# Optimization experiments

Hardware: AMD Instinct MI355X
Metric: run time of the kernel (lower is better)

## Reference

```python
import jax, jax.numpy as jnp
import numpy as np

N, E, D_IN, D_OUT, MAX_DEG = 50000, 800000, 128, 128, 64
ALPHA = 0.5


def _linear_params(key, fan_in, fan_out):
    s = 1.0 / np.sqrt(fan_in)
    kw, kb = jax.random.split(key)
    W = jax.random.uniform(kw, (fan_out, fan_in), jnp.float32, -s, s)
    b = jax.random.uniform(kb, (fan_out,), jnp.float32, -s, s)
    return W, b


def setup_inputs() -> dict:
    key = jax.random.key(0)
    ks = jax.random.split(key, 16)
    x = jax.random.normal(ks[0], (N, D_IN), jnp.float32)
    edge_index = jax.random.randint(ks[1], (2, E), 0, N, dtype=jnp.int64)
    in_degree = jax.random.randint(ks[2], (N,), 0, MAX_DEG, dtype=jnp.int64)
    out_degree = jax.random.randint(ks[3], (N,), 0, MAX_DEG, dtype=jnp.int64)
    out_deg_mask = jax.random.uniform(ks[4], (N,), jnp.float32)
    out_deg_mask_bias = jax.random.uniform(ks[5], (N,), jnp.float32)
    in_deg_mask = jax.random.uniform(ks[6], (N,), jnp.float32)
    in_deg_mask_bias = jax.random.uniform(ks[7], (N,), jnp.float32)
    W_src, b_src = _linear_params(ks[8], D_IN, D_OUT)
    W_dst, b_dst = _linear_params(ks[9], D_IN, D_OUT)
    W_out_f, b_out_f = _linear_params(ks[10], D_IN, 1)
    W_in_f, b_in_f = _linear_params(ks[11], D_IN, 1)
    W_fc, b_fc = _linear_params(ks[12], D_IN, D_OUT)
    # degree embedding tables, padding_idx=0 -> row 0 zeroed
    in_deg_table = (jax.random.normal(ks[13], (MAX_DEG, D_IN), jnp.float32)).at[0].set(0.0)
    out_deg_table = (jax.random.normal(ks[14], (MAX_DEG, D_IN), jnp.float32)).at[0].set(0.0)
    return {
        "x": x, "edge_index": edge_index,
        "in_degree": in_degree, "out_degree": out_degree,
        "out_deg_mask": out_deg_mask, "out_deg_mask_bias": out_deg_mask_bias,
        "in_deg_mask": in_deg_mask, "in_deg_mask_bias": in_deg_mask_bias,
        "W_src": W_src, "b_src": b_src, "W_dst": W_dst, "b_dst": b_dst,
        "W_out_f": W_out_f, "b_out_f": b_out_f, "W_in_f": W_in_f, "b_in_f": b_in_f,
        "W_fc": W_fc, "b_fc": b_fc,
        "in_deg_table": in_deg_table, "out_deg_table": out_deg_table,
    }


def reference(x, edge_index, in_degree, out_degree,
              out_deg_mask, out_deg_mask_bias, in_deg_mask, in_deg_mask_bias,
              W_src, b_src, W_dst, b_dst,
              W_out_f, b_out_f, W_in_f, b_in_f,
              W_fc, b_fc, in_deg_table, out_deg_table):
    n = x.shape[0]
    row, col = edge_index[0], edge_index[1]
    ones = jnp.ones(row.shape[0], x.dtype)
    # directed norm D_out^{-1/2} A D_in^{-1/2}; transpose reuses the same edge weights
    out_deg = jax.ops.segment_sum(ones, row, num_segments=n)
    in_deg = jax.ops.segment_sum(ones, col, num_segments=n)
    o_inv = jnp.where(out_deg > 0, jax.lax.rsqrt(jnp.maximum(out_deg, 1e-12)), 0.0)
    i_inv = jnp.where(in_deg > 0, jax.lax.rsqrt(jnp.maximum(in_deg, 1e-12)), 0.0)
    w = o_inv[row] * i_inv[col]  # [E]
    # adj_norm @ x and adj_t_norm @ x (SpMM via gather + segment_sum)
    out_nei = jax.ops.segment_sum(w[:, None] * x[col], row, num_segments=n)  # [N,D]
    in_nei = jax.ops.segment_sum(w[:, None] * x[row], col, num_segments=n)   # [N,D]
    # degree-gated filter
    c_out = (out_nei - x + out_deg_table[out_degree]) @ W_out_f.T + b_out_f  # [N,1]
    c_in = (in_nei - x + in_deg_table[in_degree]) @ W_in_f.T + b_in_f        # [N,1]
    C = jax.nn.softmax(jnp.concatenate([c_out, c_in], axis=1), axis=1)        # tau_softmax, tau=1
    C_out = C[:, 0:1] * out_deg_mask[:, None] + out_deg_mask_bias[:, None]
    C_in = C[:, 1:2] * in_deg_mask[:, None] + in_deg_mask_bias[:, None]
    out = (C_out * (out_nei @ W_src.T + b_src)
           + C_in * (in_nei @ W_dst.T + b_dst)
           + ALPHA * (x @ W_fc.T + b_fc))
    return out, C_in, C_out
```

## Files before the change

### kernel.cpp

```cpp
#include <hip/hip_runtime.h>

#define NN 50000
#define EE 800000
#define DD 128
#define CAP 48
#define MT 64
#define XSL 6250
#define PB 128

typedef short short8_t __attribute__((ext_vector_type(8)));
typedef float f32x4 __attribute__((ext_vector_type(4)));

__device__ __forceinline__ unsigned short f2bf(float f) {
    union { float f; unsigned int i; } v; v.f = f;
    unsigned int x = v.i;
    x += 0x7FFFu + ((x >> 16) & 1u);
    return (unsigned short)(x >> 16);
}
__device__ __forceinline__ unsigned int pack2(float a, float b) {
    return (unsigned int)f2bf(a) | ((unsigned int)f2bf(b) << 16);
}
__device__ __forceinline__ float2 bf2x2(unsigned int u) {
    union { unsigned int i; float f; } lo, hi;
    lo.i = u << 16;
    hi.i = u & 0xFFFF0000u;
    return make_float2(lo.f, hi.f);
}

__global__ void k_conv(const float* __restrict__ x,
                       const float* __restrict__ W_src,
                       const float* __restrict__ W_dst,
                       const float* __restrict__ W_fc,
                       unsigned short* __restrict__ xb,
                       unsigned short* __restrict__ wbf) {
    int t = blockIdx.x * 256 + threadIdx.x;
    int base = t * 4;
    if (base < NN * DD) {
        float4 v = *(const float4*)(x + base);
        uint2 p; p.x = pack2(v.x, v.y); p.y = pack2(v.z, v.w);
        *(uint2*)(xb + base) = p;
    } else {
        int b2 = base - NN * DD;
        if (b2 < 3 * 16384) {
            int src = b2 >> 14;
            int off = b2 & 16383;
            const float* W = (src == 0) ? W_src : (src == 1) ? W_dst : W_fc;
            float sc = (src == 2) ? 0.5f : 1.0f;
            float4 v = *(const float4*)(W + off);
            uint2 p; p.x = pack2(v.x * sc, v.y * sc); p.y = pack2(v.z * sc, v.w * sc);
            *(uint2*)(wbf + b2) = p;
        }
    }
}

__global__ void __launch_bounds__(256) k_place(
    const int* __restrict__ ei, int* __restrict__ cnt,
    unsigned short* __restrict__ bkt_row, unsigned short* __restrict__ bkt_col) {
    int xcd = blockIdx.x & 7;
    int b   = blockIdx.x >> 3;
    int lo = xcd * XSL, hi = lo + XSL;
    for (int e = b * 256 + threadIdx.x; e < EE; e += PB * 256) {
        int r = ei[e];
        int c = ei[EE + e];
        if (r >= lo && r < hi) {
            int po = atomicAdd(&cnt[r], 1);
            if (po < CAP) bkt_row[(size_t)r * CAP + po] = (unsigned short)c;
        }
        if (c >= lo && c < hi) {
            int pi = atomicAdd(&cnt[NN + c], 1);
            if (pi < CAP) bkt_col[(size_t)c * CAP + pi] = (unsigned short)r;
        }
    }
}

__global__ void k_inv(const int* __restrict__ cnt, float* __restrict__ inv) {
    int t = blockIdx.x * 256 + threadIdx.x;
    if (t >= 2 * NN) return;
    int d = cnt[t];
    inv[t] = (d > 0) ? (1.0f / sqrtf((float)d)) : 0.0f;
}

__global__ void __launch_bounds__(256) k_gather(
    const uint2* __restrict__ xb2, const float4* __restrict__ x4,
    const unsigned short* __restrict__ bkt_row, const unsigned short* __restrict__ bkt_col,
    const int* __restrict__ cnt,
    const float* __restrict__ o_inv, const float* __restrict__ i_inv,
    const int* __restrict__ in_degree, const int* __restrict__ out_degree,
    const float* __restrict__ odm, const float* __restrict__ odmb,
    const float* __restrict__ idm, const float* __restrict__ idmb,
    const float4* __restrict__ W_out_f4, const float* __restrict__ b_out_f,
    const float4* __restrict__ W_in_f4, const float* __restrict__ b_in_f,
    const float4* __restrict__ in_tab4, const float4* __restrict__ out_tab4,
    uint2* __restrict__ onb2, uint2* __restrict__ inb2,
    float* __restrict__ scbuf,
    float* __restrict__ outCin, float* __restrict__ outCout)
{
    __shared__ float4 sred[2][4][32];
    int half = threadIdx.x >> 7;
    int n = blockIdx.x * 2 + half;
    int t = threadIdx.x & 127;
    int g = t >> 5;
    int l = t & 31;

    float po_sum = 0.0f;

    float4 acc = make_float4(0.f, 0.f, 0.f, 0.f);
    {
        int deg = cnt[n]; deg = (deg > CAP) ? CAP : deg;
        const unsigned short* bp = bkt_row + (size_t)n * CAP;
        int j = g;
        for (; j + 12 < deg; j += 16) {
            int nb0 = bp[j], nb1 = bp[j + 4], nb2 = bp[j + 8], nb3 = bp[j + 12];
            float w0 = i_inv[nb0], w1 = i_inv[nb1], w2 = i_inv[nb2], w3 = i_inv[nb3];
            uint2 u0 = xb2[(size_t)nb0 * 32 + l];
            uint2 u1 = xb2[(size_t)nb1 * 32 + l];
            uint2 u2 = xb2[(size_t)nb2 * 32 + l];
            uint2 u3 = xb2[(size_t)nb3 * 32 + l];
            float2 p0 = bf2x2(u0.x), p1 = bf2x2(u0.y);
            float2 q0 = bf2x2(u1.x), q1 = bf2x2(u1.y);
            float2 r0 = bf2x2(u2.x), r1 = bf2x2(u2.y);
            float2 s0 = bf2x2(u3.x), s1 = bf2x2(u3.y);
            acc.x += w0 * p0.x + w1 * q0.x + w2 * r0.x + w3 * s0.x;
            acc.y += w0 * p0.y + w1 * q0.y + w2 * r0.y + w3 * s0.y;
            acc.z += w0 * p1.x + w1 * q1.x + w2 * r1.x + w3 * s1.x;
            acc.w += w0 * p1.y + w1 * q1.y + w2 * r1.y + w3 * s1.y;
        }
        for (; j + 4 < deg; j += 8) {
            int nb0 = bp[j], nb1 = bp[j + 4];
            float w0 = i_inv[nb0], w1 = i_inv[nb1];
            uint2 u0 = xb2[(size_t)nb0 * 32 + l];
            uint2 u1 = xb2[(size_t)nb1 * 32 + l];
            float2 p0 = bf2x2(u0.x), p1 = bf2x2(u0.y);
            float2 q0 = bf2x2(u1.x), q1 = bf2x2(u1.y);
            acc.x += w0 * p0.x + w1 * q0.x;
            acc.y += w0 * p0.y + w1 * q0.y;
            acc.z += w0 * p1.x + w1 * q1.x;
            acc.w += w0 * p1.y + w1 * q1.y;
        }
        if (j < deg) {
            int nb = bp[j];
            float w = i_inv[nb];
            uint2 u = xb2[(size_t)nb * 32 + l];
            float2 p0 = bf2x2(u.x), p1 = bf2x2(u.y);
            acc.x += w * p0.x; acc.y += w * p0.y; acc.z += w * p1.x; acc.w += w * p1.y;
        }
    }
    sred[half][g][l] = acc;
    __syncthreads();
    if (g == 0) {
        float4 a0 = sred[half][0][l], a1 = sred[half][1][l];
        float4 a2 = sred[half][2][l], a3 = sred[half][3][l];
        float wn = o_inv[n];
        float4 r;
        r.x = wn * (a0.x + a1.x + a2.x + a3.x);
        r.y = wn * (a0.y + a1.y + a2.y + a3.y);
        r.z = wn * (a0.z + a1.z + a2.z + a3.z);
        r.w = wn * (a0.w + a1.w + a2.w + a3.w);
        uint2 pw; pw.x = pack2(r.x, r.y); pw.y = pack2(r.z, r.w);
        onb2[(size_t)n * 32 + l] = pw;
        int odg = out_degree[n];
        odg = (odg < 0) ? 0 : (odg > 63 ? 63 : odg);
        float4 xv = x4[(size_t)n * 32 + l];
        float4 ot = out_tab4[(size_t)odg * 32 + l];
        float4 wf = W_out_f4[l];
        float po = (r.x - xv.x + ot.x) * wf.x + (r.y - xv.y + ot.y) * wf.y
                 + (r.z - xv.z + ot.z) * wf.z + (r.w - xv.w + ot.w) * wf.w;
        #pragma unroll
        for (int off = 16; off > 0; off >>= 1) po += __shfl_down(po, off);
        po_sum = po;
    }
    __syncthreads();

    acc = make_float4(0.f, 0.f, 0.f, 0.f);
    {
        int deg = cnt[NN + n]; deg = (deg > CAP) ? CAP : deg;
        const unsigned short* bp = bkt_col + (size_t)n * CAP;
        int j = g;
        for (; j + 12 < deg; j += 16) {
            int nb0 = bp[j], nb1 = bp[j + 4], nb2 = bp[j + 8], nb3 = bp[j + 12];
            float w0 = o_inv[nb0], w1 = o_inv[nb1], w2 = o_inv[nb2], w3 = o_inv[nb3];
            uint2 u0 = xb2[(size_t)nb0 * 32 + l];
            uint2 u1 = xb2[(size_t)nb1 * 32 + l];
            uint2 u2 = xb2[(size_t)nb2 * 32 + l];
            uint2 u3 = xb2[(size_t)nb3 * 32 + l];
            float2 p0 = bf2x2(u0.x), p1 = bf2x2(u0.y);
            float2 q0 = bf2x2(u1.x), q1 = bf2x2(u1.y);
            float2 r0 = bf2x2(u2.x), r1 = bf2x2(u2.y);
            float2 s0 = bf2x2(u3.x), s1 = bf2x2(u3.y);
            acc.x += w0 * p0.x + w1 * q0.x + w2 * r0.x + w3 * s0.x;
            acc.y += w0 * p0.y + w1 * q0.y + w2 * r0.y + w3 * s0.y;
            acc.z += w0 * p1.x + w1 * q1.x + w2 * r1.x + w3 * s1.x;
            acc.w += w0 * p1.y + w1 * q1.y + w2 * r1.y + w3 * s1.y;
        }
        for (; j + 4 < deg; j += 8) {
            int nb0 = bp[j], nb1 = bp[j + 4];
            float w0 = o_inv[nb0], w1 = o_inv[nb1];
            uint2 u0 = xb2[(size_t)nb0 * 32 + l];
            uint2 u1 = xb2[(size_t)nb1 * 32 + l];
            float2 p0 = bf2x2(u0.x), p1 = bf2x2(u0.y);
            float2 q0 = bf2x2(u1.x), q1 = bf2x2(u1.y);
            acc.x += w0 * p0.x + w1 * q0.x;
            acc.y += w0 * p0.y + w1 * q0.y;
            acc.z += w0 * p1.x + w1 * q1.x;
            acc.w += w0 * p1.y + w1 * q1.y;
        }
        if (j < deg) {
            int nb = bp[j];
            float w = o_inv[nb];
            uint2 u = xb2[(size_t)nb * 32 + l];
            float2 p0 = bf2x2(u.x), p1 = bf2x2(u.y);
            acc.x += w * p0.x; acc.y += w * p0.y; acc.z += w * p1.x; acc.w += w * p1.y;
        }
    }
    sred[half][g][l] = acc;
    __syncthreads();
    if (g == 0) {
        float4 a0 = sred[half][0][l], a1 = sred[half][1][l];
        float4 a2 = sred[half][2][l], a3 = sred[half][3][l];
        float wn = i_inv[n];
        float4 r;
        r.x = wn * (a0.x + a1.x + a2.x + a3.x);
        r.y = wn * (a0.y + a1.y + a2.y + a3.y);
        r.z = wn * (a0.z + a1.z + a2.z + a3.z);
        r.w = wn * (a0.w + a1.w + a2.w + a3.w);
        uint2 pw; pw.x = pack2(r.x, r.y); pw.y = pack2(r.z, r.w);
        inb2[(size_t)n * 32 + l] = pw;
        int idg = in_degree[n];
        idg = (idg < 0) ? 0 : (idg > 63 ? 63 : idg);
        float4 xv = x4[(size_t)n * 32 + l];
        float4 it = in_tab4[(size_t)idg * 32 + l];
        float4 wf = W_in_f4[l];
        float pi = (r.x - xv.x + it.x) * wf.x + (r.y - xv.y + it.y) * wf.y
                 + (r.z - xv.z + it.z) * wf.z + (r.w - xv.w + it.w) * wf.w;
        #pragma unroll
        for (int off = 16; off > 0; off >>= 1) pi += __shfl_down(pi, off);
        if (l == 0) {
            float c_out = po_sum + b_out_f[0];
            float c_in  = pi + b_in_f[0];
            float m  = fmaxf(c_out, c_in);
            float eo = expf(c_out - m);
            float e2 = expf(c_in  - m);
            float inv = 1.0f / (eo + e2);
            float Cout = (eo * inv) * odm[n] + odmb[n];
            float Cin  = (e2 * inv) * idm[n] + idmb[n];
            scbuf[2 * n]     = Cout;
            scbuf[2 * n + 1] = Cin;
            outCin[n]  = Cin;
            outCout[n] = Cout;
        }
    }
}

__global__ void __launch_bounds__(256) k_gemm(
    const unsigned int* __restrict__ xb32,
    const unsigned int* __restrict__ onb32, const unsigned int* __restrict__ inb32,
    const unsigned short* __restrict__ wbf,
    const float* __restrict__ b_src, const float* __restrict__ b_dst,
    const float* __restrict__ b_fc,
    const float* __restrict__ scbuf,
    float* __restrict__ out)
{
    __shared__ unsigned short sA[MT * 72];
    __shared__ unsigned short sBt[DD * 72];

    int tid = threadIdx.x;
    int wid = tid >> 6;
    int lane = tid & 63;
    int ml = lane & 15;
    int kq = lane >> 4;
    int n0 = blockIdx.x * MT;

    f32x4 accv[8];
    #pragma unroll
    for (int i = 0; i < 8; i++) accv[i] = (f32x4)0.0f;

    const unsigned int* srcs[3] = { onb32, inb32, xb32 };

    for (int kt = 0; kt < 6; kt++) {
        int srcsel = kt >> 1;
        int k0 = (kt & 1) * 64;
        const unsigned int* S = srcs[srcsel];

        #pragma unroll
        for (int r = 0; r < 2; r++) {
            int s = tid + 256 * r;
            int row = s >> 3;
            int cg = s & 7;
            int gn = n0 + row;
            uint4 p = make_uint4(0u, 0u, 0u, 0u);
            if (gn < NN) {
                uint4 u = *(const uint4*)(S + (size_t)gn * 64 + (k0 >> 1) + cg * 4);
                if (srcsel == 2) {
                    p = u;
                } else {
                    float sc = scbuf[2 * gn + srcsel];
                    float2 a = bf2x2(u.x), b = bf2x2(u.y), c = bf2x2(u.z), d = bf2x2(u.w);
                    p.x = pack2(a.x * sc, a.y * sc);
                    p.y = pack2(b.x * sc, b.y * sc);
                    p.z = pack2(c.x * sc, c.y * sc);
                    p.w = pack2(d.x * sc, d.y * sc);
                }
            }
            *(uint4*)(sA + row * 72 + cg * 8) = p;
        }
        #pragma unroll
        for (int r = 0; r < 4; r++) {
            int s = tid + 256 * r;
            int row = s >> 3;
            int cg = s & 7;
            uint4 w = *(const uint4*)(wbf + srcsel * 16384 + row * DD + k0 + cg * 8);
            *(uint4*)(sBt + row * 72 + cg * 8) = w;
        }
        __syncthreads();

        #pragma unroll
        for (int ks = 0; ks < 64; ks += 32) {
            short8_t a = *(const short8_t*)(sA + (16 * wid + ml) * 72 + ks + kq * 8);
            #pragma unroll
            for (int i = 0; i < 8; i++) {
                short8_t b = *(const short8_t*)(sBt + (16 * i + ml) * 72 + ks + kq * 8);
                accv[i] = __builtin_amdgcn_mfma_f32_16x16x32_bf16(a, b, accv[i], 0, 0, 0);
            }
        }
        __syncthreads();
    }

    int row_base = n0 + 16 * wid + 4 * kq;
    #pragma unroll
    for (int r = 0; r < 4; r++) {
        int row = row_base + r;
        if (row >= NN) continue;
        float Cout = scbuf[2 * row];
        float Cin  = scbuf[2 * row + 1];
        #pragma unroll
        for (int i = 0; i < 8; i++) {
            int col = 16 * i + ml;
            out[(size_t)row * DD + col] =
                accv[i][r] + Cout * b_src[col] + Cin * b_dst[col] + 0.5f * b_fc[col];
        }
    }
}

extern "C" void kernel_launch(void* const* d_in, const int* in_sizes, int n_in,
                              void* d_out, int out_size, void* d_ws, size_t ws_size,
                              hipStream_t stream) {
    const float* x    = (const float*)d_in[0];
    const int* ei     = (const int*)d_in[1];
    const int* in_degree  = (const int*)d_in[2];
    const int* out_degree = (const int*)d_in[3];
    const float* odm  = (const float*)d_in[4];
    const float* odmb = (const float*)d_in[5];
    const float* idm  = (const float*)d_in[6];
    const float* idmb = (const float*)d_in[7];
    const float* W_src = (const float*)d_in[8];
    const float* b_src = (const float*)d_in[9];
    const float* W_dst = (const float*)d_in[10];
    const float* b_dst = (const float*)d_in[11];
    const float* W_out_f = (const float*)d_in[12];
    const float* b_out_f = (const float*)d_in[13];
    const float* W_in_f  = (const float*)d_in[14];
    const float* b_in_f  = (const float*)d_in[15];
    const float* W_fc    = (const float*)d_in[16];
    const float* b_fc    = (const float*)d_in[17];
    const float* in_tab  = (const float*)d_in[18];
    const float* out_tab = (const float*)d_in[19];

    unsigned short* xb  = (unsigned short*)d_ws;
    unsigned short* onb = xb + (size_t)NN * DD;
    unsigned short* inb = onb + (size_t)NN * DD;
    float* scbuf = (float*)(inb + (size_t)NN * DD);
    float* invb  = scbuf + 2 * NN;
    unsigned short* wbf = (unsigned short*)(invb + 2 * NN);
    int* cnt     = (int*)(wbf + 3 * 16384);
    unsigned short* bkt_row = (unsigned short*)(cnt + 2 * NN);
    unsigned short* bkt_col = bkt_row + (size_t)NN * CAP;

    hipMemsetAsync(cnt, 0, (size_t)2 * NN * sizeof(int), stream);

    int conv_quads = (NN * DD + 3 * 16384) / 4;
    k_conv<<<(conv_quads + 255) / 256, 256, 0, stream>>>(x, W_src, W_dst, W_fc, xb, wbf);
    k_place<<<8 * PB, 256, 0, stream>>>(ei, cnt, bkt_row, bkt_col);
    k_inv<<<(2 * NN + 255) / 256, 256, 0, stream>>>(cnt, invb);

    float* o_inv = invb;
    float* i_inv = invb + NN;
    float* out_p  = (float*)d_out;
    float* cin_p  = out_p + (size_t)NN * DD;
    float* cout_p = cin_p + NN;

    k_gather<<<NN / 2, 256, 0, stream>>>((const uint2*)xb, (const float4*)x,
                                         bkt_row, bkt_col, cnt,
                                         o_inv, i_inv, in_degree, out_degree,
                                         odm, odmb, idm, idmb,
                                         (const float4*)W_out_f, b_out_f,
                                         (const float4*)W_in_f, b_in_f,
                                         (const float4*)in_tab, (const float4*)out_tab,
                                         (uint2*)onb, (uint2*)inb,
                                         scbuf, cin_p, cout_p);

    k_gemm<<<(NN + MT - 1) / MT, 256, 0, stream>>>(
        (const unsigned int*)xb, (const unsigned int*)onb, (const unsigned int*)inb,
        wbf, b_src, b_dst, b_fc, scbuf, out_p);
}
```

Before: 297.7 us.

## Gather both edge directions concurrently and pre-scale neighbor sums by gates

The gather kernel now gives two warp-groups to each direction (out-neighbors and in-neighbors) so both SpMM gathers run at once instead of one after the other, with deeper unrolling to keep eight loads in flight. The softmax gates are computed in shared memory and applied to the aggregated rows before the bf16 store. The GEMM loader can then copy the A tiles straight through without unpacking, scaling and repacking. The gather has more syncs and less per-group parallelism within each direction, and the gate scaling now happens before bf16 rounding instead of after, which changes rounding slightly.

```diff
diff --git a/kernel.cpp b/kernel.cpp
--- a/kernel.cpp
+++ b/kernel.cpp
@@ -96,158 +96,140 @@
     float* __restrict__ outCin, float* __restrict__ outCout)
 {
     __shared__ float4 sred[2][4][32];
+    __shared__ float sg[2][2];
+    __shared__ float sC[2][2];
     int half = threadIdx.x >> 7;
     int n = blockIdx.x * 2 + half;
     int t = threadIdx.x & 127;
     int g = t >> 5;
     int l = t & 31;
-
-    float po_sum = 0.0f;
+    int dir = g >> 1;
+    int gd  = g & 1;
+
+    const unsigned short* bp = ((dir == 0) ? bkt_row : bkt_col) + (size_t)n * CAP;
+    const float* wnb = (dir == 0) ? i_inv : o_inv;
+    int deg = cnt[dir * NN + n]; deg = (deg > CAP) ? CAP : deg;
 
     float4 acc = make_float4(0.f, 0.f, 0.f, 0.f);
-    {
-        int deg = cnt[n]; deg = (deg > CAP) ? CAP : deg;
-        const unsigned short* bp = bkt_row + (size_t)n * CAP;
-        int j = g;
-        for (; j + 12 < deg; j += 16) {
-            int nb0 = bp[j], nb1 = bp[j + 4], nb2 = bp[j + 8], nb3 = bp[j + 12];
-            float w0 = i_inv[nb0], w1 = i_inv[nb1], w2 = i_inv[nb2], w3 = i_inv[nb3];
-            uint2 u0 = xb2[(size_t)nb0 * 32 + l];
-            uint2 u1 = xb2[(size_t)nb1 * 32 + l];
-            uint2 u2 = xb2[(size_t)nb2 * 32 + l];
-            uint2 u3 = xb2[(size_t)nb3 * 32 + l];
-            float2 p0 = bf2x2(u0.x), p1 = bf2x2(u0.y);
-            float2 q0 = bf2x2(u1.x), q1 = bf2x2(u1.y);
-            float2 r0 = bf2x2(u2.x), r1 = bf2x2(u2.y);
-            float2 s0 = bf2x2(u3.x), s1 = bf2x2(u3.y);
-            acc.x += w0 * p0.x + w1 * q0.x + w2 * r0.x + w3 * s0.x;
-            acc.y += w0 * p0.y + w1 * q0.y + w2 * r0.y + w3 * s0.y;
-            acc.z += w0 * p1.x + w1 * q1.x + w2 * r1.x + w3 * s1.x;
-            acc.w += w0 * p1.y + w1 * q1.y + w2 * r1.y + w3 * s1.y;
-        }
-        for (; j + 4 < deg; j += 8) {
-            int nb0 = bp[j], nb1 = bp[j + 4];
-            float w0 = i_inv[nb0], w1 = i_inv[nb1];
-            uint2 u0 = xb2[(size_t)nb0 * 32 + l];
-            uint2 u1 = xb2[(size_t)nb1 * 32 + l];
-            float2 p0 = bf2x2(u0.x), p1 = bf2x2(u0.y);
-            float2 q0 = bf2x2(u1.x), q1 = bf2x2(u1.y);
-            acc.x += w0 * p0.x + w1 * q0.x;
-            acc.y += w0 * p0.y + w1 * q0.y;
-            acc.z += w0 * p1.x + w1 * q1.x;
-            acc.w += w0 * p1.y + w1 * q1.y;
-        }
-        if (j < deg) {
-            int nb = bp[j];
-            float w = i_inv[nb];
-            uint2 u = xb2[(size_t)nb * 32 + l];
-            float2 p0 = bf2x2(u.x), p1 = bf2x2(u.y);
-            acc.x += w * p0.x; acc.y += w * p0.y; acc.z += w * p1.x; acc.w += w * p1.y;
-        }
-    }
+    int j = gd;
+    for (; j + 14 < deg; j += 16) {
+        int nb0 = bp[j],      nb1 = bp[j + 2],  nb2_ = bp[j + 4],  nb3 = bp[j + 6];
+        int nb4 = bp[j + 8],  nb5 = bp[j + 10], nb6 = bp[j + 12],  nb7 = bp[j + 14];
+        float w0 = wnb[nb0], w1 = wnb[nb1], w2 = wnb[nb2_], w3 = wnb[nb3];
+        float w4 = wnb[nb4], w5 = wnb[nb5], w6 = wnb[nb6],  w7 = wnb[nb7];
+        uint2 u0 = xb2[(size_t)nb0 * 32 + l];
+        uint2 u1 = xb2[(size_t)nb1 * 32 + l];
+        uint2 u2 = xb2[(size_t)nb2_ * 32 + l];
+        uint2 u3 = xb2[(size_t)nb3 * 32 + l];
+        uint2 u4 = xb2[(size_t)nb4 * 32 + l];
+        uint2 u5 = xb2[(size_t)nb5 * 32 + l];
+        uint2 u6 = xb2[(size_t)nb6 * 32 + l];
+        uint2 u7 = xb2[(size_t)nb7 * 32 + l];
+        float2 p0 = bf2x2(u0.x), p1 = bf2x2(u0.y);
+        float2 q0 = bf2x2(u1.x), q1 = bf2x2(u1.y);
+        float2 r0 = bf2x2(u2.x), r1 = bf2x2(u2.y);
+        float2 s0 = bf2x2(u3.x), s1 = bf2x2(u3.y);
+        float2 t0 = bf2x2(u4.x), t1 = bf2x2(u4.y);
+        float2 v0 = bf2x2(u5.x), v1 = bf2x2(u5.y);
+        float2 y0 = bf2x2(u6.x), y1 = bf2x2(u6.y);
+        float2 z0 = bf2x2(u7.x), z1 = bf2x2(u7.y);
+        acc.x += w0 * p0.x + w1 * q0.x + w2 * r0.x + w3 * s0.x
+               + w4 * t0.x + w5 * v0.x + w6 * y0.x + w7 * z0.x;
+        acc.y += w0 * p0.y + w1 * q0.y + w2 * r0.y + w3 * s0.y
+               + w4 * t0.y + w5 * v0.y + w6 * y0.y + w7 * z0.y;
+        acc.z += w0 * p1.x + w1 * q1.x + w2 * r1.x + w3 * s1.x
+               + w4 * t1.x + w5 * v1.x + w6 * y1.x + w7 * z1.x;
+        acc.w += w0 * p1.y + w1 * q1.y + w2 * r1.y + w3 * s1.y
+               + w4 * t1.y + w5 * v1.y + w6 * y1.y + w7 * z1.y;
+    }
+    for (; j + 6 < deg; j += 8) {
+        int nb0 = bp[j], nb1 = bp[j + 2], nb2_ = bp[j + 4], nb3 = bp[j + 6];
+        float w0 = wnb[nb0], w1 = wnb[nb1], w2 = wnb[nb2_], w3 = wnb[nb3];
+        uint2 u0 = xb2[(size_t)nb0 * 32 + l];
+        uint2 u1 = xb2[(size_t)nb1 * 32 + l];
+        uint2 u2 = xb2[(size_t)nb2_ * 32 + l];
+        uint2 u3 = xb2[(size_t)nb3 * 32 + l];
+        float2 p0 = bf2x2(u0.x), p1 = bf2x2(u0.y);
+        float2 q0 = bf2x2(u1.x), q1 = bf2x2(u1.y);
+        float2 r0 = bf2x2(u2.x), r1 = bf2x2(u2.y);
+        float2 s0 = bf2x2(u3.x), s1 = bf2x2(u3.y);
+        acc.x += w0 * p0.x + w1 * q0.x + w2 * r0.x + w3 * s0.x;
+        acc.y += w0 * p0.y + w1 * q0.y + w2 * r0.y + w3 * s0.y;
+        acc.z += w0 * p1.x + w1 * q1.x + w2 * r1.x + w3 * s1.x;
+        acc.w += w0 * p1.y + w1 * q1.y + w2 * r1.y + w3 * s1.y;
+    }
+    for (; j + 2 < deg; j += 4) {
+        int nb0 = bp[j], nb1 = bp[j + 2];
+        float w0 = wnb[nb0], w1 = wnb[nb1];
+        uint2 u0 = xb2[(size_t)nb0 * 32 + l];
+        uint2 u1 = xb2[(size_t)nb1 * 32 + l];
+        float2 p0 = bf2x2(u0.x), p1 = bf2x2(u0.y);
+        float2 q0 = bf2x2(u1.x), q1 = bf2x2(u1.y);
+        acc.x += w0 * p0.x + w1 * q0.x;
+        acc.y += w0 * p0.y + w1 * q0.y;
+        acc.z += w0 * p1.x + w1 * q1.x;
+        acc.w += w0 * p1.y + w1 * q1.y;
+    }
+    if (j < deg) {
+        int nb = bp[j];
+        float w = wnb[nb];
+        uint2 u = xb2[(size_t)nb * 32 + l];
+        float2 p0 = bf2x2(u.x), p1 = bf2x2(u.y);
+        acc.x += w * p0.x; acc.y += w * p0.y; acc.z += w * p1.x; acc.w += w * p1.y;
+    }
+
     sred[half][g][l] = acc;
     __syncthreads();
-    if (g == 0) {
-        float4 a0 = sred[half][0][l], a1 = sred[half][1][l];
-        float4 a2 = sred[half][2][l], a3 = sred[half][3][l];
-        float wn = o_inv[n];
-        float4 r;
-        r.x = wn * (a0.x + a1.x + a2.x + a3.x);
-        r.y = wn * (a0.y + a1.y + a2.y + a3.y);
-        r.z = wn * (a0.z + a1.z + a2.z + a3.z);
-        r.w = wn * (a0.w + a1.w + a2.w + a3.w);
-        uint2 pw; pw.x = pack2(r.x, r.y); pw.y = pack2(r.z, r.w);
-        onb2[(size_t)n * 32 + l] = pw;
-        int odg = out_degree[n];
-        odg = (odg < 0) ? 0 : (odg > 63 ? 63 : odg);
+
+    float4 r = make_float4(0.f, 0.f, 0.f, 0.f);
+    if (gd == 0) {
+        float4 a0 = sred[half][dir * 2][l];
+        float4 a1 = sred[half][dir * 2 + 1][l];
+        float wn = (dir == 0) ? o_inv[n] : i_inv[n];
+        r.x = wn * (a0.x + a1.x);
+        r.y = wn * (a0.y + a1.y);
+        r.z = wn * (a0.z + a1.z);
+        r.w = wn * (a0.w + a1.w);
         float4 xv = x4[(size_t)n * 32 + l];
-        float4 ot = out_tab4[(size_t)odg * 32 + l];
-        float4 wf = W_out_f4[l];
-        float po = (r.x - xv.x + ot.x) * wf.x + (r.y - xv.y + ot.y) * wf.y
-                 + (r.z - xv.z + ot.z) * wf.z + (r.w - xv.w + ot.w) * wf.w;
-        #pragma unroll
-        for (int off = 16; off > 0; off >>= 1) po += __shfl_down(po, off);
-        po_sum = po;
+        float4 tb, wf;
+        if (dir == 0) {
+            int odg = out_degree[n];
+            odg = (odg < 0) ? 0 : (odg > 63 ? 63 : odg);
+            tb = out_tab4[(size_t)odg * 32 + l];
+            wf = W_out_f4[l];
+        } else {
+            int idg = in_degree[n];
+            idg = (idg < 0) ? 0 : (idg > 63 ? 63 : idg);
+            tb = in_tab4[(size_t)idg * 32 + l];
+            wf = W_in_f4[l];
+        }
+        float p = (r.x - xv.x + tb.x) * wf.x + (r.y - xv.y + tb.y) * wf.y
+                + (r.z - xv.z + tb.z) * wf.z + (r.w - xv.w + tb.w) * wf.w;
+        #pragma unroll
+        for (int off = 16; off > 0; off >>= 1) p += __shfl_down(p, off);
+        if (l == 0) sg[half][dir] = p;
     }
     __syncthreads();
-
-    acc = make_float4(0.f, 0.f, 0.f, 0.f);
-    {
-        int deg = cnt[NN + n]; deg = (deg > CAP) ? CAP : deg;
-        const unsigned short* bp = bkt_col + (size_t)n * CAP;
-        int j = g;
-        for (; j + 12 < deg; j += 16) {
-            int nb0 = bp[j], nb1 = bp[j + 4], nb2 = bp[j + 8], nb3 = bp[j + 12];
-            float w0 = o_inv[nb0], w1 = o_inv[nb1], w2 = o_inv[nb2], w3 = o_inv[nb3];
-            uint2 u0 = xb2[(size_t)nb0 * 32 + l];
-            uint2 u1 = xb2[(size_t)nb1 * 32 + l];
-            uint2 u2 = xb2[(size_t)nb2 * 32 + l];
-            uint2 u3 = xb2[(size_t)nb3 * 32 + l];
-            float2 p0 = bf2x2(u0.x), p1 = bf2x2(u0.y);
-            float2 q0 = bf2x2(u1.x), q1 = bf2x2(u1.y);
-            float2 r0 = bf2x2(u2.x), r1 = bf2x2(u2.y);
-            float2 s0 = bf2x2(u3.x), s1 = bf2x2(u3.y);
-            acc.x += w0 * p0.x + w1 * q0.x + w2 * r0.x + w3 * s0.x;
-            acc.y += w0 * p0.y + w1 * q0.y + w2 * r0.y + w3 * s0.y;
-            acc.z += w0 * p1.x + w1 * q1.x + w2 * r1.x + w3 * s1.x;
-            acc.w += w0 * p1.y + w1 * q1.y + w2 * r1.y + w3 * s1.y;
-        }
-        for (; j + 4 < deg; j += 8) {
-            int nb0 = bp[j], nb1 = bp[j + 4];
-            float w0 = o_inv[nb0], w1 = o_inv[nb1];
-            uint2 u0 = xb2[(size_t)nb0 * 32 + l];
-            uint2 u1 = xb2[(size_t)nb1 * 32 + l];
-            float2 p0 = bf2x2(u0.x), p1 = bf2x2(u0.y);
-            float2 q0 = bf2x2(u1.x), q1 = bf2x2(u1.y);
-            acc.x += w0 * p0.x + w1 * q0.x;
-            acc.y += w0 * p0.y + w1 * q0.y;
-            acc.z += w0 * p1.x + w1 * q1.x;
-            acc.w += w0 * p1.y + w1 * q1.y;
-        }
-        if (j < deg) {
-            int nb = bp[j];
-            float w = o_inv[nb];
-            uint2 u = xb2[(size_t)nb * 32 + l];
-            float2 p0 = bf2x2(u.x), p1 = bf2x2(u.y);
-            acc.x += w * p0.x; acc.y += w * p0.y; acc.z += w * p1.x; acc.w += w * p1.y;
-        }
-    }
-    sred[half][g][l] = acc;
+    if (t == 0) {
+        float c_out = sg[half][0] + b_out_f[0];
+        float c_in  = sg[half][1] + b_in_f[0];
+        float m  = fmaxf(c_out, c_in);
+        float eo = expf(c_out - m);
+        float e2 = expf(c_in  - m);
+        float inv = 1.0f / (eo + e2);
+        float Cout = (eo * inv) * odm[n] + odmb[n];
+        float Cin  = (e2 * inv) * idm[n] + idmb[n];
+        sC[half][0] = Cout; sC[half][1] = Cin;
+        scbuf[2 * n]     = Cout;
+        scbuf[2 * n + 1] = Cin;
+        outCout[n] = Cout;
+        outCin[n]  = Cin;
+    }
     __syncthreads();
-    if (g == 0) {
-        float4 a0 = sred[half][0][l], a1 = sred[half][1][l];
-        float4 a2 = sred[half][2][l], a3 = sred[half][3][l];
-        float wn = i_inv[n];
-        float4 r;
-        r.x = wn * (a0.x + a1.x + a2.x + a3.x);
-        r.y = wn * (a0.y + a1.y + a2.y + a3.y);
-        r.z = wn * (a0.z + a1.z + a2.z + a3.z);
-        r.w = wn * (a0.w + a1.w + a2.w + a3.w);
-        uint2 pw; pw.x = pack2(r.x, r.y); pw.y = pack2(r.z, r.w);
-        inb2[(size_t)n * 32 + l] = pw;
-        int idg = in_degree[n];
-        idg = (idg < 0) ? 0 : (idg > 63 ? 63 : idg);
-        float4 xv = x4[(size_t)n * 32 + l];
-        float4 it = in_tab4[(size_t)idg * 32 + l];
-        float4 wf = W_in_f4[l];
-        float pi = (r.x - xv.x + it.x) * wf.x + (r.y - xv.y + it.y) * wf.y
-                 + (r.z - xv.z + it.z) * wf.z + (r.w - xv.w + it.w) * wf.w;
-        #pragma unroll
-        for (int off = 16; off > 0; off >>= 1) pi += __shfl_down(pi, off);
-        if (l == 0) {
-            float c_out = po_sum + b_out_f[0];
-            float c_in  = pi + b_in_f[0];
-            float m  = fmaxf(c_out, c_in);
-            float eo = expf(c_out - m);
-            float e2 = expf(c_in  - m);
-            float inv = 1.0f / (eo + e2);
-            float Cout = (eo * inv) * odm[n] + odmb[n];
-            float Cin  = (e2 * inv) * idm[n] + idmb[n];
-            scbuf[2 * n]     = Cout;
-            scbuf[2 * n + 1] = Cin;
-            outCin[n]  = Cin;
-            outCout[n] = Cout;
-        }
+    if (gd == 0) {
+        float C = sC[half][dir];
+        uint2 pw; pw.x = pack2(C * r.x, C * r.y); pw.y = pack2(C * r.z, C * r.w);
+        ((dir == 0) ? onb2 : inb2)[(size_t)n * 32 + l] = pw;
     }
 }
 
@@ -289,17 +271,7 @@
             int gn = n0 + row;
             uint4 p = make_uint4(0u, 0u, 0u, 0u);
             if (gn < NN) {
-                uint4 u = *(const uint4*)(S + (size_t)gn * 64 + (k0 >> 1) + cg * 4);
-                if (srcsel == 2) {
-                    p = u;
-                } else {
-                    float sc = scbuf[2 * gn + srcsel];
-                    float2 a = bf2x2(u.x), b = bf2x2(u.y), c = bf2x2(u.z), d = bf2x2(u.w);
-                    p.x = pack2(a.x * sc, a.y * sc);
-                    p.y = pack2(b.x * sc, b.y * sc);
-                    p.z = pack2(c.x * sc, c.y * sc);
-                    p.w = pack2(d.x * sc, d.y * sc);
-                }
+                p = *(const uint4*)(S + (size_t)gn * 64 + (k0 >> 1) + cg * 4);
             }
             *(uint4*)(sA + row * 72 + cg * 8) = p;
         }
```

Measured after the change: 292.0 us. No clear change (-1.9%).
